# Performance work log

Hardware: AMD Instinct MI355X
Metric: run time of the kernel (lower is better)

## Reference

```python
import jax, jax.numpy as jnp
import numpy as np

B, S, D, H, HD, L, V = 32, 512, 512, 8, 64, 6, 64000
EPS = 1e-5

def _layer_norm(x, g, b):
    mu = jnp.mean(x, axis=-1, keepdims=True)
    var = jnp.mean(jnp.square(x - mu), axis=-1, keepdims=True)
    return (x - mu) * jax.lax.rsqrt(var + EPS) * g + b

def _sinusoidal_pe():
    pos = np.arange(S)[:, None].astype(np.float32)
    div = np.exp(np.arange(0, D, 2).astype(np.float32) * -(np.log(10000.0) / D))
    pe = np.zeros((S, D), dtype=np.float32)
    pe[:, 0::2] = np.sin(pos * div)
    pe[:, 1::2] = np.cos(pos * div)
    return jnp.asarray(pe)

def setup_inputs() -> dict:
    key = jax.random.key(0)
    ks = jax.random.split(key, 8)
    std = 0.02
    return {
        'tokens': jax.random.randint(ks[0], (B, S), 0, V),
        'mask': jnp.ones((B, S), dtype=jnp.int32),
        'emb': jax.random.normal(ks[1], (V, D), jnp.float32) * std,
        'pe': _sinusoidal_pe(),
        'Wq': jax.random.normal(ks[2], (L, H, D, HD), jnp.float32) * std,
        'Wk': jax.random.normal(ks[3], (L, H, D, HD), jnp.float32) * std,
        'Wv': jax.random.normal(ks[4], (L, H, D, HD), jnp.float32) * std,
        'Wo': jax.random.normal(ks[5], (L, D, D), jnp.float32) * std,
        'ln1_g': jnp.ones((L, D), jnp.float32),
        'ln1_b': jnp.zeros((L, D), jnp.float32),
        'W1': jax.random.normal(ks[6], (L, D, 4 * D), jnp.float32) * std,
        'b1': jnp.zeros((L, 4 * D), jnp.float32),
        'W2': jax.random.normal(ks[7], (L, 4 * D, D), jnp.float32) * std,
        'b2': jnp.zeros((L, D), jnp.float32),
        'ln2_g': jnp.ones((L, D), jnp.float32),
        'ln2_b': jnp.zeros((L, D), jnp.float32),
    }

def reference(tokens, mask, emb, pe, Wq, Wk, Wv, Wo, ln1_g, ln1_b, W1, b1, W2, b2, ln2_g, ln2_b):
    # Eval mode: all dropouts are identity.
    x = emb[tokens] + pe[None, :S, :]               # [B,S,D]
    neg_inf = jnp.finfo(x.dtype).min
    mask_b = (mask == 0)[:, None, None, :]          # [B,1,1,S] broadcast over heads & queries
    scale = HD ** -0.5
    for l in range(L):
        q = jnp.einsum('bsd,hde->bhse', x, Wq[l])
        k = jnp.einsum('bsd,hde->bhse', x, Wk[l])
        v = jnp.einsum('bsd,hde->bhse', x, Wv[l])
        w = jnp.einsum('bhse,bhte->bhst', q, k) * scale
        w = jnp.where(mask_b, neg_inf, w)
        a = jax.nn.softmax(w, axis=-1)
        o = jnp.einsum('bhst,bhte->bhse', a, v)     # [B,H,S,HD]
        o = o.transpose(0, 2, 1, 3).reshape(x.shape[0], S, D)  # concat heads
        x = _layer_norm(x + o @ Wo[l], ln1_g[l], ln1_b[l])
        h = jax.nn.gelu(x @ W1[l] + b1[l], approximate=False) @ W2[l] + b2[l]
        x = _layer_norm(x + h, ln2_g[l], ln2_b[l])
    return x
```

## Files before the change

kernel.cpp:

```cpp
#include <hip/hip_runtime.h>

#define BB 32
#define SS 512
#define DD 512
#define HH 8
#define HDH 64
#define LL 6
#define DFF 2048
#define MM (BB*SS)

typedef __attribute__((ext_vector_type(4))) float f32x4;
typedef __attribute__((ext_vector_type(8))) short s16x8;
typedef __attribute__((ext_vector_type(4))) short s16x4;

__device__ __forceinline__ unsigned short f2bf(float f) {
    union { float f; unsigned u; } v; v.f = f;
    unsigned r = v.u + 0x7fffu + ((v.u >> 16) & 1u);
    return (unsigned short)(r >> 16);
}
__device__ __forceinline__ float bf2f(unsigned short b) {
    union { unsigned u; float f; } v; v.u = ((unsigned)b) << 16;
    return v.f;
}
__device__ __forceinline__ float exp2_fast(float x) {
    float r; asm("v_exp_f32 %0, %1" : "=v"(r) : "v"(x)); return r;
}

__device__ __forceinline__ f32x4 mfma_bf16(s16x8 a, s16x8 b, f32x4 c) {
    asm("v_mfma_f32_16x16x32_bf16 %0, %1, %2, %0" : "+v"(c) : "v"(a), "v"(b));
    return c;
}

__device__ __forceinline__ void gload_lds16(const void* g, void* l) {
    __builtin_amdgcn_global_load_lds(
        (__attribute__((address_space(1))) void*)g,
        (__attribute__((address_space(3))) void*)l, 16, 0, 0);
}

__device__ __forceinline__ void tile_transpose_conv(
    const float* __restrict__ src, int srcPitch,
    unsigned short* __restrict__ dst, int dstPitch,
    float* lt, float scale)
{
    const int t = threadIdx.x;
    #pragma unroll
    for (int it = 0; it < 4; ++it) {
        int r = it * 16 + (t >> 4);
        int c = (t & 15) * 4;
        f32x4 v = *(const f32x4*)(src + (size_t)r * srcPitch + c);
        lt[r * 65 + c + 0] = v[0];
        lt[r * 65 + c + 1] = v[1];
        lt[r * 65 + c + 2] = v[2];
        lt[r * 65 + c + 3] = v[3];
    }
    __syncthreads();
    int nn = t >> 2;
    int kc = (t & 3) * 16;
    s16x8 o0, o1;
    #pragma unroll
    for (int i = 0; i < 8; ++i)  o0[i] = (short)f2bf(lt[(kc + i) * 65 + nn] * scale);
    #pragma unroll
    for (int i = 0; i < 8; ++i)  o1[i] = (short)f2bf(lt[(kc + 8 + i) * 65 + nn] * scale);
    *(s16x8*)(dst + (size_t)nn * dstPitch + kc) = o0;
    *(s16x8*)(dst + (size_t)nn * dstPitch + kc + 8) = o1;
}

__global__ __launch_bounds__(256) void k_tconv_all(
    const float* __restrict__ Wq, const float* __restrict__ Wk,
    const float* __restrict__ Wv, const float* __restrict__ Wo,
    const float* __restrict__ W1, const float* __restrict__ W2,
    unsigned short* __restrict__ wqkv_t, unsigned short* __restrict__ wo_t,
    unsigned short* __restrict__ w1_t, unsigned short* __restrict__ w2_t)
{
    __shared__ float lt[64 * 65];
    int bid = blockIdx.x;
    if (bid < 1152) {
        int which = bid / 384;
        int rem = bid - which * 384;
        int l = rem >> 6;
        int h = (rem >> 3) & 7;
        int kt = rem & 7;
        const float* W = which == 0 ? Wq : (which == 1 ? Wk : Wv);
        float scale = (which == 1) ? 0.18033688011116048f : 1.0f;
        const float* srcT = W + (((size_t)(l * HH + h) * 512) + kt * 64) * 64;
        unsigned short* dstT = wqkv_t + ((size_t)l * 1536 + which * 512 + h * 64) * 512 + kt * 64;
        tile_transpose_conv(srcT, 64, dstT, 512, lt, scale);
        return;
    }
    const float* src; unsigned short* dst; int K, N, rem;
    if (bid < 1536)      { src = Wo; dst = wo_t; K = 512;  N = 512;  rem = bid - 1152; }
    else if (bid < 3072) { src = W1; dst = w1_t; K = 512;  N = 2048; rem = bid - 1536; }
    else                 { src = W2; dst = w2_t; K = 2048; N = 512;  rem = bid - 3072; }
    int tpb = (K >> 6) * (N >> 6);
    int l = rem / tpb;
    int r2 = rem - l * tpb;
    int kt = r2 / (N >> 6);
    int ntile = r2 - kt * (N >> 6);
    const float* srcT = src + (size_t)l * K * N + (size_t)(kt * 64) * N + ntile * 64;
    unsigned short* dstT = dst + (size_t)l * N * K + (size_t)(ntile * 64) * K + kt * 64;
    tile_transpose_conv(srcT, N, dstT, K, lt, 1.0f);
}

__global__ __launch_bounds__(256) void k_embed(const int* __restrict__ tokens,
                                               const float* __restrict__ emb,
                                               const float* __restrict__ pe,
                                               unsigned short* __restrict__ xh,
                                               unsigned short* __restrict__ xl) {
    int i = blockIdx.x * 256 + threadIdx.x;
    int row = i >> 7;
    int d4 = (i & 127) * 4;
    int srow = row & (SS - 1);
    int tok = tokens[row];
    f32x4 ev = *(const f32x4*)(emb + (size_t)tok*DD + d4);
    f32x4 pv = *(const f32x4*)(pe + (size_t)srow*DD + d4);
    s16x4 hv, lv;
    #pragma unroll
    for (int j = 0; j < 4; ++j) {
        float v = ev[j] + pv[j];
        unsigned short hi = f2bf(v);
        hv[j] = (short)hi;
        lv[j] = (short)f2bf(v - bf2f(hi));
    }
    *(s16x4*)(xh + (size_t)row*DD + d4) = hv;
    *(s16x4*)(xl + (size_t)row*DD + d4) = lv;
}

__global__ __launch_bounds__(128) void k_ln(unsigned short* xh,
                                            unsigned short* xl,
                                            const unsigned short* __restrict__ y,
                                            const float* __restrict__ gg,
                                            const float* __restrict__ bb,
                                            float* __restrict__ xo) {
    const int row = blockIdx.x;
    const int tid = threadIdx.x;
    __shared__ float red[4];
    s16x4 hv0 = *(const s16x4*)(xh + (size_t)row*DD + tid*4);
    s16x4 lv0 = *(const s16x4*)(xl + (size_t)row*DD + tid*4);
    s16x4 yv = *(const s16x4*)(y + (size_t)row*DD + tid*4);
    f32x4 vv;
    #pragma unroll
    for (int j = 0; j < 4; ++j)
        vv[j] = (bf2f((unsigned short)hv0[j]) + bf2f((unsigned short)lv0[j]))
                + bf2f((unsigned short)yv[j]);
    float sum = vv[0] + vv[1] + vv[2] + vv[3];
    #pragma unroll
    for (int off = 1; off < 64; off <<= 1) sum += __shfl_xor(sum, off);
    if ((tid & 63) == 0) red[tid >> 6] = sum;
    __syncthreads();
    float mu = (red[0] + red[1]) * (1.0f / 512.0f);
    float s2 = 0.0f;
    #pragma unroll
    for (int j = 0; j < 4; ++j) { float d = vv[j] - mu; s2 += d * d; }
    #pragma unroll
    for (int off = 1; off < 64; off <<= 1) s2 += __shfl_xor(s2, off);
    if ((tid & 63) == 0) red[2 + (tid >> 6)] = s2;
    __syncthreads();
    float var = (red[2] + red[3]) * (1.0f / 512.0f);
    float rs = rsqrtf(var + 1e-5f);
    f32x4 gv = *(const f32x4*)(gg + tid*4);
    f32x4 bv = *(const f32x4*)(bb + tid*4);
    s16x4 hv, lv;
    f32x4 ov;
    #pragma unroll
    for (int j = 0; j < 4; ++j) {
        float o = (vv[j] - mu) * rs * gv[j] + bv[j];
        ov[j] = o;
        unsigned short hi = f2bf(o);
        hv[j] = (short)hi;
        lv[j] = (short)f2bf(o - bf2f(hi));
    }
    *(s16x4*)(xh + (size_t)row*DD + tid*4) = hv;
    *(s16x4*)(xl + (size_t)row*DD + tid*4) = lv;
    if (xo) *(f32x4*)(xo + (size_t)row*DD + tid*4) = ov;
}

template<int EPI>
__global__ __launch_bounds__(256, 2) void k_gemm(
    const unsigned short* __restrict__ A, const unsigned short* __restrict__ Bt,
    unsigned short* __restrict__ ob,
    const float* __restrict__ bias, int N, int K, int nt)
{
    __shared__ short lds[2][2][4096];
    const int tid = threadIdx.x;
    const int lane = tid & 63;
    const int wid = tid >> 6;
    const int g = lane >> 4;
    const int t16 = lane & 15;

    int nwg = gridDim.x;
    int bid = blockIdx.x;
    int cpx = nwg >> 3;
    int swz = (bid & 7) * cpx + (bid >> 3);
    int bm = swz / nt;
    int bn = swz - bm * nt;

    const unsigned short* Ag = A  + (size_t)bm * 128 * K;
    const unsigned short* Bg = Bt + (size_t)bn * 128 * K;

    auto stage = [&](int buf, int k0) {
        #pragma unroll
        for (int i = 0; i < 2; ++i) {
            int slot = i * 256 + tid;
            int r = slot >> 2;
            int j = slot & 3;
            int js = j ^ ((r >> 1) & 3);
            size_t go = (size_t)r * K + k0 + js * 8;
            int lo = i * 2048 + wid * 512;
            gload_lds16(Ag + go, &lds[buf][0][lo]);
            gload_lds16(Bg + go, &lds[buf][1][lo]);
        }
    };

    f32x4 acc[4][4];
    #pragma unroll
    for (int a_ = 0; a_ < 4; ++a_)
        #pragma unroll
        for (int b_ = 0; b_ < 4; ++b_) acc[a_][b_] = (f32x4){0.f, 0.f, 0.f, 0.f};

    const int wm = wid >> 1, wn = wid & 1;
    stage(0, 0);
    __syncthreads();
    int nk = K >> 5;
    int buf = 0;
    for (int kt = 0; kt < nk; ++kt) {
        if (kt + 1 < nk) stage(buf ^ 1, (kt + 1) << 5);
        s16x8 af[4], bf_[4];
        #pragma unroll
        for (int mt = 0; mt < 4; ++mt) {
            int r = wm * 64 + mt * 16 + t16;
            af[mt] = *(const s16x8*)&lds[buf][0][r * 32 + ((g ^ ((r >> 1) & 3)) << 3)];
        }
        #pragma unroll
        for (int nt_ = 0; nt_ < 4; ++nt_) {
            int r = wn * 64 + nt_ * 16 + t16;
            bf_[nt_] = *(const s16x8*)&lds[buf][1][r * 32 + ((g ^ ((r >> 1) & 3)) << 3)];
        }
        #pragma unroll
        for (int mt = 0; mt < 4; ++mt)
            #pragma unroll
            for (int nt_ = 0; nt_ < 4; ++nt_)
                acc[mt][nt_] = mfma_bf16(af[mt], bf_[nt_], acc[mt][nt_]);
        __syncthreads();
        buf ^= 1;
    }

    #pragma unroll
    for (int mt = 0; mt < 4; ++mt)
        #pragma unroll
        for (int nt_ = 0; nt_ < 4; ++nt_) {
            int row0 = bm * 128 + wm * 64 + mt * 16 + g * 4;
            int col  = bn * 128 + wn * 64 + nt_ * 16 + t16;
            f32x4 v = acc[mt][nt_];
            float bv = (EPI == 2) ? bias[col] : 0.0f;
            #pragma unroll
            for (int r_ = 0; r_ < 4; ++r_) {
                size_t idx = (size_t)(row0 + r_) * N + col;
                if (EPI == 0) {
                    ob[idx] = f2bf(v[r_]);
                } else {
                    float tv = v[r_] + bv;
                    float ge = 0.5f * tv * (1.0f + erff(tv * 0.70710678118f));
                    ob[idx] = f2bf(ge);
                }
            }
        }
}

__global__ __launch_bounds__(512, 2) void k_gemm8(
    const unsigned short* __restrict__ A, const unsigned short* __restrict__ Bt,
    unsigned short* __restrict__ ob,
    const float* __restrict__ bias, int N, int K, int nt)
{
    extern __shared__ short lds[];
    const int tid = threadIdx.x;
    const int lane = tid & 63;
    const int wid = tid >> 6;
    const int g = lane >> 4;
    const int t16 = lane & 15;
    const int wm = wid >> 2, wn = wid & 3;

    int nwg = gridDim.x;
    int bid = blockIdx.x;
    int cpx = nwg >> 3;
    int swz = (bid & 7) * cpx + (bid >> 3);
    int bm = swz / nt;
    int bn = swz - bm * nt;

    const unsigned short* Ag = A  + (size_t)bm * 256 * K;
    const unsigned short* Bg = Bt + (size_t)bn * 128 * K;

    auto stage_unit = [&](int slot, int t, int unit) {
        const int k0 = t << 6;
        const unsigned short* src = (unit == 2) ? Bg : (Ag + (unit ? (size_t)128 * K : 0));
        short* dst0 = lds + slot * 24576 + (unit == 2 ? 16384 : unit * 8192);
        #pragma unroll
        for (int rr = 0; rr < 2; ++rr) {
            int rb = rr * 64 + wid * 8;
            int r_in = rb + (lane >> 3);
            int c = (lane & 7) ^ (r_in & 7);
            gload_lds16(src + (size_t)r_in * K + k0 + c * 8, dst0 + rb * 64);
        }
    };

    f32x4 acc[8][2];
    #pragma unroll
    for (int a_ = 0; a_ < 8; ++a_)
        #pragma unroll
        for (int b_ = 0; b_ < 2; ++b_) acc[a_][b_] = (f32x4){0.f, 0.f, 0.f, 0.f};

    const int nk = K >> 6;
    stage_unit(0, 0, 0); stage_unit(0, 0, 1); stage_unit(0, 0, 2);
    stage_unit(1, 1, 0); stage_unit(1, 1, 1); stage_unit(1, 1, 2);

    int slot = 0;
    for (int t = 0; t < nk; ++t) {
        if (t + 1 < nk) asm volatile("s_waitcnt vmcnt(6)" ::: "memory");
        else            asm volatile("s_waitcnt vmcnt(0)" ::: "memory");
        __builtin_amdgcn_s_barrier();
        __builtin_amdgcn_sched_barrier(0);

        int s2 = slot + 2; if (s2 >= 3) s2 -= 3;
        const short* As = lds + slot * 24576;
        const short* Bs = As + 16384;

        if (t + 2 < nk) { stage_unit(s2, t + 2, 0); stage_unit(s2, t + 2, 1); }
        s16x8 bfr[2][2];
        #pragma unroll
        for (int nn = 0; nn < 2; ++nn) {
            int row = wn * 32 + nn * 16 + t16;
            #pragma unroll
            for (int kk = 0; kk < 2; ++kk)
                bfr[nn][kk] = *(const s16x8*)&Bs[row * 64 + (((kk * 4 + g) ^ (row & 7)) << 3)];
        }
        {
            s16x8 afr[4][2];
            #pragma unroll
            for (int mm = 0; mm < 4; ++mm) {
                int row = wm * 128 + mm * 16 + t16;
                #pragma unroll
                for (int kk = 0; kk < 2; ++kk)
                    afr[mm][kk] = *(const s16x8*)&As[row * 64 + (((kk * 4 + g) ^ (row & 7)) << 3)];
            }
            __builtin_amdgcn_sched_barrier(0);
            __builtin_amdgcn_s_setprio(1);
            #pragma unroll
            for (int mm = 0; mm < 4; ++mm)
                #pragma unroll
                for (int nn = 0; nn < 2; ++nn)
                    #pragma unroll
                    for (int kk = 0; kk < 2; ++kk)
                        acc[mm][nn] = mfma_bf16(afr[mm][kk], bfr[nn][kk], acc[mm][nn]);
            __builtin_amdgcn_s_setprio(0);
            __builtin_amdgcn_sched_barrier(0);
        }
        if (t + 2 < nk) stage_unit(s2, t + 2, 2);
        {
            s16x8 afr[4][2];
            #pragma unroll
            for (int mm = 0; mm < 4; ++mm) {
                int row = wm * 128 + (mm + 4) * 16 + t16;
                #pragma unroll
                for (int kk = 0; kk < 2; ++kk)
                    afr[mm][kk] = *(const s16x8*)&As[row * 64 + (((kk * 4 + g) ^ (row & 7)) << 3)];
            }
            __builtin_amdgcn_sched_barrier(0);
            __builtin_amdgcn_s_setprio(1);
            #pragma unroll
            for (int mm = 0; mm < 4; ++mm)
                #pragma unroll
                for (int nn = 0; nn < 2; ++nn)
                    #pragma unroll
                    for (int kk = 0; kk < 2; ++kk)
                        acc[mm + 4][nn] = mfma_bf16(afr[mm][kk], bfr[nn][kk], acc[mm + 4][nn]);
            __builtin_amdgcn_s_setprio(0);
            __builtin_amdgcn_sched_barrier(0);
        }
        slot = slot + 1 == 3 ? 0 : slot + 1;
    }

    #pragma unroll
    for (int mm = 0; mm < 8; ++mm)
        #pragma unroll
        for (int nn = 0; nn < 2; ++nn) {
            int row0 = bm * 256 + wm * 128 + mm * 16 + g * 4;
            int col  = bn * 128 + wn * 32 + nn * 16 + t16;
            f32x4 v = acc[mm][nn];
            float bv = bias[col];
            #pragma unroll
            for (int r_ = 0; r_ < 4; ++r_)
                ob[(size_t)(row0 + r_) * N + col] = f2bf(v[r_] + bv);
        }
}

__global__ __launch_bounds__(1024, 4) void k_attn(
    const unsigned short* __restrict__ qkv, const int* __restrict__ mask,
    unsigned short* __restrict__ o)
{
    extern __shared__ short smem[];
    short* Kl = smem;
    short* Vl = smem + 32768;
    const int tid = threadIdx.x;
    const int lane = tid & 63, wid = tid >> 6;
    short* Pl = smem + 65536 + wid * 1024;
    const int b = blockIdx.x >> 3, h = blockIdx.x & 7;
    const unsigned short* base = qkv + (size_t)b * SS * 1536;
    const int qc = h * 64, kc = 512 + h * 64, vc = 1024 + h * 64;

    {
        int row0 = (tid >> 3);
        int s = tid & 7;
        #pragma unroll
        for (int it = 0; it < 4; ++it) {
            int row = it * 128 + row0;
            int j = s ^ (row & 7);
            gload_lds16(base + (size_t)row * 1536 + kc + j * 8,
                        Kl + it * 8192 + wid * 512);
        }
    }
    {
        int unit = tid >> 1, half = tid & 1;
        int t0 = (unit >> 3) << 3, e0 = (unit & 7) << 3;
        s16x8 r0 = *(const s16x8*)(base + (size_t)(t0 + half*4 + 0) * 1536 + vc + e0);
        s16x8 r1 = *(const s16x8*)(base + (size_t)(t0 + half*4 + 1) * 1536 + vc + e0);
        s16x8 r2 = *(const s16x8*)(base + (size_t)(t0 + half*4 + 2) * 1536 + vc + e0);
        s16x8 r3 = *(const s16x8*)(base + (size_t)(t0 + half*4 + 3) * 1536 + vc + e0);
        #pragma unroll
        for (int j = 0; j < 8; ++j) {
            int e = e0 + j;
            int slot = (t0 >> 3) ^ (e & 7) ^ ((e >> 3) & 7);
            s16x4 w = (s16x4){r0[j], r1[j], r2[j], r3[j]};
            *(s16x4*)(Vl + e * 512 + (slot << 3) + (half << 2)) = w;
        }
    }
    const int g = lane >> 4, t16 = lane & 15;
    unsigned mbits = 0;
    for (int n2 = 0; n2 < 32; ++n2)
        if (mask[b * SS + n2 * 16 + t16] != 0) mbits |= (1u << n2);
    __syncthreads();

    for (int qi = 0; qi < 2; ++qi) {
        const int q0 = (wid * 2 + qi) * 16;
        s16x8 aq[2];
        #pragma unroll
        for (int ks = 0; ks < 2; ++ks)
            aq[ks] = *(const s16x8*)(base + (size_t)(q0 + t16) * 1536 + qc + ks * 32 + g * 8);

        f32x4 oacc[4];
        #pragma unroll
        for (int eo = 0; eo < 4; ++eo) oacc[eo] = (f32x4){0.f, 0.f, 0.f, 0.f};
        float mx[4] = {-3.0e38f, -3.0e38f, -3.0e38f, -3.0e38f};
        float ls[4] = {0.f, 0.f, 0.f, 0.f};

        for (int tc = 0; tc < 4; ++tc) {
            f32x4 s[8];
            #pragma unroll
            for (int n2 = 0; n2 < 8; ++n2) s[n2] = (f32x4){0.f, 0.f, 0.f, 0.f};
            #pragma unroll
            for (int n2 = 0; n2 < 8; ++n2) {
                int t = tc * 128 + n2 * 16 + t16;
                #pragma unroll
                for (int ks = 0; ks < 2; ++ks) {
                    int blk = ks * 4 + g;
                    s16x8 bk = *(const s16x8*)(Kl + t * 64 + ((blk ^ (t & 7)) << 3));
                    s[n2] = mfma_bf16(aq[ks], bk, s[n2]);
                }
            }
            #pragma unroll
            for (int n2 = 0; n2 < 8; ++n2) {
                bool val = (mbits >> (tc * 8 + n2)) & 1u;
                #pragma unroll
                for (int r_ = 0; r_ < 4; ++r_)
                    s[n2][r_] = val ? s[n2][r_] : -3.0e38f;
            }
            float sc[4];
            #pragma unroll
            for (int r_ = 0; r_ < 4; ++r_) {
                float m = s[0][r_];
                #pragma unroll
                for (int n2 = 1; n2 < 8; ++n2) m = fmaxf(m, s[n2][r_]);
                #pragma unroll
                for (int off = 1; off < 16; off <<= 1) m = fmaxf(m, __shfl_xor(m, off));
                float mn = fmaxf(mx[r_], m);
                sc[r_] = exp2_fast(mx[r_] - mn);
                mx[r_] = mn;
                ls[r_] *= sc[r_];
            }
            #pragma unroll
            for (int eo = 0; eo < 4; ++eo)
                #pragma unroll
                for (int r_ = 0; r_ < 4; ++r_) oacc[eo][r_] *= sc[r_];
            #pragma unroll
            for (int n2 = 0; n2 < 8; ++n2)
                #pragma unroll
                for (int r_ = 0; r_ < 4; ++r_)
                    s[n2][r_] = exp2_fast(s[n2][r_] - mx[r_]);
            #pragma unroll
            for (int r_ = 0; r_ < 4; ++r_) {
                float t = 0.f;
                #pragma unroll
                for (int n2 = 0; n2 < 8; ++n2) t += s[n2][r_];
                #pragma unroll
                for (int off = 1; off < 16; off <<= 1) t += __shfl_xor(t, off);
                ls[r_] += t;
            }
            #pragma unroll
            for (int c4 = 0; c4 < 2; ++c4) {
                #pragma unroll
                for (int k4 = 0; k4 < 4; ++k4) {
                    int n2 = c4 * 4 + k4;
                    #pragma unroll
                    for (int r_ = 0; r_ < 4; ++r_) {
                        int qq = g * 4 + r_;
                        int kk = k4 * 16 + t16;
                        Pl[qq * 64 + (((kk >> 3) ^ (qq & 7)) << 3) + (kk & 7)] =
                            (short)f2bf(s[n2][r_]);
                    }
                }
                #pragma unroll
                for (int ks2 = 0; ks2 < 2; ++ks2) {
                    int kk = ks2 * 32 + g * 8;
                    s16x8 pa = *(const s16x8*)(Pl + t16 * 64 + (((kk >> 3) ^ (t16 & 7)) << 3));
                    int tg = tc * 128 + c4 * 64 + kk;
                    #pragma unroll
                    for (int eo = 0; eo < 4; ++eo) {
                        int e = eo * 16 + t16;
                        int slot = (tg >> 3) ^ (e & 7) ^ ((e >> 3) & 7);
                        s16x8 bv = *(const s16x8*)(Vl + e * 512 + (slot << 3));
                        oacc[eo] = mfma_bf16(pa, bv, oacc[eo]);
                    }
                }
            }
        }
        #pragma unroll
        for (int eo = 0; eo < 4; ++eo)
            #pragma unroll
            for (int r_ = 0; r_ < 4; ++r_) {
                int row = q0 + g * 4 + r_;
                int e = eo * 16 + t16;
                o[((size_t)b * SS + row) * DD + h * HDH + e] =
                    f2bf(oacc[eo][r_] / ls[r_]);
            }
    }
}

extern "C" void kernel_launch(void* const* d_in, const int* in_sizes, int n_in,
                              void* d_out, int out_size, void* d_ws, size_t ws_size,
                              hipStream_t stream)
{
    const int*   tokens = (const int*)d_in[0];
    const int*   mask   = (const int*)d_in[1];
    const float* emb    = (const float*)d_in[2];
    const float* pe     = (const float*)d_in[3];
    const float* Wq     = (const float*)d_in[4];
    const float* Wk     = (const float*)d_in[5];
    const float* Wv     = (const float*)d_in[6];
    const float* Wo     = (const float*)d_in[7];
    const float* l1g    = (const float*)d_in[8];
    const float* l1b    = (const float*)d_in[9];
    const float* W1     = (const float*)d_in[10];
    const float* b1     = (const float*)d_in[11];
    const float* W2     = (const float*)d_in[12];
    const float* b2     = (const float*)d_in[13];
    const float* l2g    = (const float*)d_in[14];
    const float* l2b    = (const float*)d_in[15];

    char* p = (char*)d_ws;
    auto alloc = [&](size_t bytes) { char* r = p; p += (bytes + 255) & ~(size_t)255; return r; };
    unsigned short* wqkv_t = (unsigned short*)alloc((size_t)LL*3*DD*DD*2);
    unsigned short* wo_t   = (unsigned short*)alloc((size_t)LL*DD*DD*2);
    unsigned short* w1_t   = (unsigned short*)alloc((size_t)LL*DD*DFF*2);
    unsigned short* w2_t   = (unsigned short*)alloc((size_t)LL*DD*DFF*2);
    unsigned short* xh     = (unsigned short*)alloc((size_t)MM*DD*2);
    unsigned short* xl     = (unsigned short*)alloc((size_t)MM*DD*2);
    unsigned short* qkvb   = (unsigned short*)alloc((size_t)MM*1536*2);
    unsigned short* obuf   = (unsigned short*)alloc((size_t)MM*DD*2);
    unsigned short* ybufb  = (unsigned short*)alloc((size_t)MM*DD*2);
    unsigned short* hbuf   = qkvb;

    k_tconv_all<<<4608, 256, 0, stream>>>(Wq, Wk, Wv, Wo, W1, W2,
                                          wqkv_t, wo_t, w1_t, w2_t);
    k_embed<<<8192, 256, 0, stream>>>(tokens, emb, pe, xh, xl);

    hipFuncSetAttribute((const void*)k_attn,
                        hipFuncAttributeMaxDynamicSharedMemorySize, 163840);
    hipFuncSetAttribute((const void*)k_gemm8,
                        hipFuncAttributeMaxDynamicSharedMemorySize, 147456);

    for (int l = 0; l < LL; ++l) {
        const unsigned short* wqkvl = wqkv_t + (size_t)l*3*DD*DD;
        const unsigned short* wol   = wo_t   + (size_t)l*DD*DD;
        const unsigned short* w1l   = w1_t   + (size_t)l*DD*DFF;
        const unsigned short* w2l   = w2_t   + (size_t)l*DD*DFF;

        k_gemm<0><<<1536, 256, 0, stream>>>(xh, wqkvl, qkvb, nullptr, 1536, 512, 12);
        k_attn<<<256, 1024, 163840, stream>>>(qkvb, mask, obuf);
        k_gemm<0><<<512, 256, 0, stream>>>(obuf, wol, ybufb, nullptr, 512, 512, 4);
        k_ln<<<16384, 128, 0, stream>>>(xh, xl, ybufb, l1g + l*DD, l1b + l*DD, nullptr);
        k_gemm<2><<<2048, 256, 0, stream>>>(xh, w1l, hbuf, b1 + (size_t)l*DFF, 2048, 512, 16);
        k_gemm8<<<256, 512, 147456, stream>>>(hbuf, w2l, ybufb, b2 + (size_t)l*DD, 512, 2048, 4);
        float* xout = (l == LL - 1) ? (float*)d_out : nullptr;
        k_ln<<<16384, 128, 0, stream>>>(xh, xl, ybufb, l2g + l*DD, l2b + l*DD, xout);
    }
}
```

Baseline: 1.336 ms.

## Split attention over key halves and query halves with a merge kernel

Attention blocks now each handle one (batch, head, query-half, key-half) tile, giving 1024 blocks of 512 threads with half the LDS instead of 256 blocks of 1024 threads. Each block writes unnormalized partial outputs plus per-row max and sum, and a new merge kernel combines the two key halves with log-sum-exp rescaling. This targets low occupancy and poor CU fill on a 256-block grid. In exchange it adds a partial-output round trip through global memory, an extra launch per layer, and rounds the partials to bf16 before they are merged.

```diff
diff --git a/kernel.cpp b/kernel.cpp
--- a/kernel.cpp
+++ b/kernel.cpp
@@ -392,54 +392,60 @@
         }
 }
 
-__global__ __launch_bounds__(1024, 4) void k_attn(
+__global__ __launch_bounds__(512, 4) void k_attn(
     const unsigned short* __restrict__ qkv, const int* __restrict__ mask,
-    unsigned short* __restrict__ o)
+    unsigned short* __restrict__ op, float* __restrict__ mbuf,
+    float* __restrict__ lbuf)
 {
     extern __shared__ short smem[];
     short* Kl = smem;
-    short* Vl = smem + 32768;
+    short* Vl = smem + 16384;
     const int tid = threadIdx.x;
     const int lane = tid & 63, wid = tid >> 6;
-    short* Pl = smem + 65536 + wid * 1024;
-    const int b = blockIdx.x >> 3, h = blockIdx.x & 7;
+    short* Pl = smem + 32768 + wid * 1024;
+    const int kh = blockIdx.x & 1;
+    const int qh = (blockIdx.x >> 1) & 1;
+    const int h  = (blockIdx.x >> 2) & 7;
+    const int b  = blockIdx.x >> 5;
     const unsigned short* base = qkv + (size_t)b * SS * 1536;
     const int qc = h * 64, kc = 512 + h * 64, vc = 1024 + h * 64;
+    const int k0g = kh * 256;
 
     {
-        int row0 = (tid >> 3);
+        int row0 = tid >> 3;
         int s = tid & 7;
         #pragma unroll
         for (int it = 0; it < 4; ++it) {
-            int row = it * 128 + row0;
+            int row = it * 64 + row0;
             int j = s ^ (row & 7);
-            gload_lds16(base + (size_t)row * 1536 + kc + j * 8,
-                        Kl + it * 8192 + wid * 512);
+            gload_lds16(base + (size_t)(k0g + row) * 1536 + kc + j * 8,
+                        Kl + it * 4096 + wid * 512);
         }
     }
     {
         int unit = tid >> 1, half = tid & 1;
-        int t0 = (unit >> 3) << 3, e0 = (unit & 7) << 3;
-        s16x8 r0 = *(const s16x8*)(base + (size_t)(t0 + half*4 + 0) * 1536 + vc + e0);
-        s16x8 r1 = *(const s16x8*)(base + (size_t)(t0 + half*4 + 1) * 1536 + vc + e0);
-        s16x8 r2 = *(const s16x8*)(base + (size_t)(t0 + half*4 + 2) * 1536 + vc + e0);
-        s16x8 r3 = *(const s16x8*)(base + (size_t)(t0 + half*4 + 3) * 1536 + vc + e0);
+        int t0 = (unit >> 3) << 3;
+        int e0 = (unit & 7) << 3;
+        s16x8 r0 = *(const s16x8*)(base + (size_t)(k0g + t0 + half*4 + 0) * 1536 + vc + e0);
+        s16x8 r1 = *(const s16x8*)(base + (size_t)(k0g + t0 + half*4 + 1) * 1536 + vc + e0);
+        s16x8 r2 = *(const s16x8*)(base + (size_t)(k0g + t0 + half*4 + 2) * 1536 + vc + e0);
+        s16x8 r3 = *(const s16x8*)(base + (size_t)(k0g + t0 + half*4 + 3) * 1536 + vc + e0);
         #pragma unroll
         for (int j = 0; j < 8; ++j) {
             int e = e0 + j;
             int slot = (t0 >> 3) ^ (e & 7) ^ ((e >> 3) & 7);
             s16x4 w = (s16x4){r0[j], r1[j], r2[j], r3[j]};
-            *(s16x4*)(Vl + e * 512 + (slot << 3) + (half << 2)) = w;
+            *(s16x4*)(Vl + e * 256 + (slot << 3) + (half << 2)) = w;
         }
     }
     const int g = lane >> 4, t16 = lane & 15;
     unsigned mbits = 0;
-    for (int n2 = 0; n2 < 32; ++n2)
-        if (mask[b * SS + n2 * 16 + t16] != 0) mbits |= (1u << n2);
+    for (int n2 = 0; n2 < 16; ++n2)
+        if (mask[b * SS + k0g + n2 * 16 + t16] != 0) mbits |= (1u << n2);
     __syncthreads();
 
     for (int qi = 0; qi < 2; ++qi) {
-        const int q0 = (wid * 2 + qi) * 16;
+        const int q0 = qh * 256 + (wid * 2 + qi) * 16;
         s16x8 aq[2];
         #pragma unroll
         for (int ks = 0; ks < 2; ++ks)
@@ -451,7 +457,7 @@
         float mx[4] = {-3.0e38f, -3.0e38f, -3.0e38f, -3.0e38f};
         float ls[4] = {0.f, 0.f, 0.f, 0.f};
 
-        for (int tc = 0; tc < 4; ++tc) {
+        for (int tc = 0; tc < 2; ++tc) {
             f32x4 s[8];
             #pragma unroll
             for (int n2 = 0; n2 < 8; ++n2) s[n2] = (f32x4){0.f, 0.f, 0.f, 0.f};
@@ -525,7 +531,7 @@
                     for (int eo = 0; eo < 4; ++eo) {
                         int e = eo * 16 + t16;
                         int slot = (tg >> 3) ^ (e & 7) ^ ((e >> 3) & 7);
-                        s16x8 bv = *(const s16x8*)(Vl + e * 512 + (slot << 3));
+                        s16x8 bv = *(const s16x8*)(Vl + e * 256 + (slot << 3));
                         oacc[eo] = mfma_bf16(pa, bv, oacc[eo]);
                     }
                 }
@@ -537,10 +543,46 @@
             for (int r_ = 0; r_ < 4; ++r_) {
                 int row = q0 + g * 4 + r_;
                 int e = eo * 16 + t16;
-                o[((size_t)b * SS + row) * DD + h * HDH + e] =
-                    f2bf(oacc[eo][r_] / ls[r_]);
-            }
-    }
+                op[(size_t)kh * MM * DD + ((size_t)b * SS + row) * DD + h * HDH + e] =
+                    f2bf(oacc[eo][r_]);
+            }
+        if (t16 == 0) {
+            #pragma unroll
+            for (int r_ = 0; r_ < 4; ++r_) {
+                int row = q0 + g * 4 + r_;
+                size_t u = (size_t)kh * MM * HH + ((size_t)b * SS + row) * HH + h;
+                mbuf[u] = mx[r_];
+                lbuf[u] = ls[r_];
+            }
+        }
+    }
+}
+
+__global__ __launch_bounds__(256) void k_attn_merge(
+    const unsigned short* __restrict__ op, const float* __restrict__ mbuf,
+    const float* __restrict__ lbuf, unsigned short* __restrict__ o)
+{
+    int i = blockIdx.x * 256 + threadIdx.x;
+    int eq = i & 15;
+    int unit = i >> 4;
+    int h = unit & 7;
+    int brow = unit >> 3;
+    float m0 = mbuf[unit], m1 = mbuf[MM * HH + unit];
+    float l0 = lbuf[unit], l1 = lbuf[MM * HH + unit];
+    float ms = fmaxf(m0, m1);
+    float w0 = exp2_fast(m0 - ms);
+    float w1 = exp2_fast(m1 - ms);
+    float inv = 1.0f / (l0 * w0 + l1 * w1);
+    w0 *= inv; w1 *= inv;
+    size_t off = (size_t)brow * DD + h * HDH + eq * 4;
+    s16x4 a = *(const s16x4*)(op + off);
+    s16x4 c = *(const s16x4*)(op + (size_t)MM * DD + off);
+    s16x4 r;
+    #pragma unroll
+    for (int j = 0; j < 4; ++j)
+        r[j] = (short)f2bf(bf2f((unsigned short)a[j]) * w0 +
+                           bf2f((unsigned short)c[j]) * w1);
+    *(s16x4*)(o + off) = r;
 }
 
 extern "C" void kernel_launch(void* const* d_in, const int* in_sizes, int n_in,
@@ -575,6 +617,9 @@
     unsigned short* qkvb   = (unsigned short*)alloc((size_t)MM*1536*2);
     unsigned short* obuf   = (unsigned short*)alloc((size_t)MM*DD*2);
     unsigned short* ybufb  = (unsigned short*)alloc((size_t)MM*DD*2);
+    unsigned short* opart  = (unsigned short*)alloc((size_t)2*MM*DD*2);
+    float*          mbuf   = (float*)alloc((size_t)2*MM*HH*4);
+    float*          lbuf   = (float*)alloc((size_t)2*MM*HH*4);
     unsigned short* hbuf   = qkvb;
 
     k_tconv_all<<<4608, 256, 0, stream>>>(Wq, Wk, Wv, Wo, W1, W2,
@@ -582,7 +627,7 @@
     k_embed<<<8192, 256, 0, stream>>>(tokens, emb, pe, xh, xl);
 
     hipFuncSetAttribute((const void*)k_attn,
-                        hipFuncAttributeMaxDynamicSharedMemorySize, 163840);
+                        hipFuncAttributeMaxDynamicSharedMemorySize, 81920);
     hipFuncSetAttribute((const void*)k_gemm8,
                         hipFuncAttributeMaxDynamicSharedMemorySize, 147456);
 
@@ -593,7 +638,8 @@
         const unsigned short* w2l   = w2_t   + (size_t)l*DD*DFF;
 
         k_gemm<0><<<1536, 256, 0, stream>>>(xh, wqkvl, qkvb, nullptr, 1536, 512, 12);
-        k_attn<<<256, 1024, 163840, stream>>>(qkvb, mask, obuf);
+        k_attn<<<1024, 512, 81920, stream>>>(qkvb, mask, opart, mbuf, lbuf);
+        k_attn_merge<<<8192, 256, 0, stream>>>(opart, mbuf, lbuf, obuf);
         k_gemm<0><<<512, 256, 0, stream>>>(obuf, wol, ybufb, nullptr, 512, 512, 4);
         k_ln<<<16384, 128, 0, stream>>>(xh, xl, ybufb, l1g + l*DD, l1b + l*DD, nullptr);
         k_gemm<2><<<2048, 256, 0, stream>>>(xh, w1l, hbuf, b1 + (size_t)l*DFF, 2048, 512, 16);
```

Result: slower. 1.419 ms (+6.2%).
